# Kernel tuning notes

Hardware: AMD Instinct MI355X
Metric: run time of the kernel (lower is better)

The kernel has to match this reference:

```python
import jax, jax.numpy as jnp
import numpy as np
from jax.scipy.special import gammaln

LOG_PROBS_PRECISION = -1.0e5  # large negative log-prob for impossible obs under bookend state
N_STATES_TOTAL = 25           # 1 bookend + 24 NB states
N_SPOTS = 4_000_000
TOTAL_EXP_READ_DEPTH = 25.0


def setup_inputs() -> dict:
    key = jax.random.key(0)
    k1, k2, k3 = jax.random.split(key, 3)
    # init_emission: means = depth * rand, phis = rand
    state_means = TOTAL_EXP_READ_DEPTH * jax.random.uniform(k1, (N_STATES_TOTAL,), dtype=jnp.float32)
    state_phis = jax.random.uniform(k2, (N_STATES_TOTAL,), dtype=jnp.float32)
    obs = jax.random.randint(k3, (N_SPOTS,), 0, 50, dtype=jnp.int32)
    return {"state_means": state_means, "state_phis": state_phis, "obs": obs}


def reference(state_means, state_phis, obs):
    # obs: [S] int counts -> float for lgamma math
    x = obs.astype(jnp.float32)  # [S]
    # Bookend state (index 0): log_prob 0 where obs == 0, else LOG_PROBS_PRECISION
    bookend = jnp.where(obs > 0, jnp.float32(LOG_PROBS_PRECISION), jnp.float32(0.0))  # [S]
    # NB states 1..K: mean/overdispersion parameterization
    mu = state_means[1:, None]   # [K, 1]
    phi = state_phis[1:, None]   # [K, 1]
    nb = (gammaln(x[None, :] + phi) - gammaln(phi) - gammaln(x[None, :] + 1.0)
          + phi * jnp.log(phi / (phi + mu))
          + x[None, :] * jnp.log(mu / (phi + mu)))  # [K, S]
    return jnp.concatenate([bookend[None, :], nb], axis=0)  # [K+1, S]
```

## Files before the change

### kernel.cpp

```cpp
#include <hip/hip_runtime.h>
#include <hip/hip_bf16.h>

#define N_STATES 25
#define N_XVALS  50
#define TBL_SZ   (N_STATES * N_XVALS)
#define LOG_PROBS_PRECISION -100000.0f

typedef int   i32x4 __attribute__((ext_vector_type(4)));
typedef float f32x4 __attribute__((ext_vector_type(4)));

__global__ void build_table_kernel(const float* __restrict__ means,
                                   const float* __restrict__ phis,
                                   float* __restrict__ table) {
    int idx = blockIdx.x * blockDim.x + threadIdx.x;
    if (idx >= TBL_SZ) return;
    int s = idx / N_XVALS;
    int x = idx % N_XVALS;
    float v;
    if (s == 0) {
        v = (x > 0) ? LOG_PROBS_PRECISION : 0.0f;
    } else {
        float mu  = means[s];
        float phi = phis[s];
        float rising = 0.0f;
        for (int j = 0; j < x; ++j) rising += logf(phi + (float)j);
        float logfact = 0.0f;
        for (int j = 2; j <= x; ++j) logfact += logf((float)j);
        float c = phi * logf(phi / (phi + mu));
        float d = logf(mu  / (phi + mu));
        v = rising - logfact + c + (float)x * d;
    }
    table[idx] = v;
}

__global__ __launch_bounds__(256) void
emit_kernel(const int* __restrict__ obs,
            const float* __restrict__ table,
            float* __restrict__ out,
            int n_spots) {
    __shared__ float t[TBL_SZ];
    for (int i = threadIdx.x; i < TBL_SZ; i += 256) t[i] = table[i];
    __syncthreads();

    int g = blockIdx.x * 256 + threadIdx.x;
    if (g * 4 >= n_spots) return;

    i32x4 o = __builtin_nontemporal_load(((const i32x4*)obs) + g);
    int x0 = min(max(o.x, 0), N_XVALS - 1);
    int x1 = min(max(o.y, 0), N_XVALS - 1);
    int x2 = min(max(o.z, 0), N_XVALS - 1);
    int x3 = min(max(o.w, 0), N_XVALS - 1);

#pragma unroll
    for (int s = 0; s < N_STATES; ++s) {
        const float* row = t + s * N_XVALS;
        f32x4 v;
        v.x = row[x0];
        v.y = row[x1];
        v.z = row[x2];
        v.w = row[x3];
        f32x4* dst = ((f32x4*)(out + (size_t)s * (size_t)n_spots)) + g;
        __builtin_nontemporal_store(v, dst);
    }
}

extern "C" void kernel_launch(void* const* d_in, const int* in_sizes, int n_in,
                              void* d_out, int out_size, void* d_ws, size_t ws_size,
                              hipStream_t stream) {
    const float* means = (const float*)d_in[0];
    const float* phis  = (const float*)d_in[1];
    const int*   obs   = (const int*)d_in[2];
    float* out = (float*)d_out;
    float* table = (float*)d_ws;

    int n_spots = in_sizes[2];

    build_table_kernel<<<(TBL_SZ + 255) / 256, 256, 0, stream>>>(means, phis, table);

    int groups = n_spots / 4;
    int blocks = (groups + 255) / 256;
    emit_kernel<<<blocks, 256, 0, stream>>>(obs, table, out, n_spots);
}
```

Before: 414.4 us.

## Split emission gather into per-state grid rows, each block writing one output row

The emit kernel now uses a 2D grid with one grid row per state, so each block writes a contiguous chunk of a single output row. Each block handles 1024 groups of four spots and loads only its 50-entry table row into shared memory. The goal is more streaming, locality-friendly writes and a smaller shared-memory footprint. In exchange, obs is read 25 times instead of once (about 400 MB of output plus repeated 16 MB input reads), and the nontemporal load hint on obs is dropped so those reads can hit in cache.

```diff
diff --git a/kernel.cpp b/kernel.cpp
--- a/kernel.cpp
+++ b/kernel.cpp
@@ -5,6 +5,7 @@
 #define N_XVALS  50
 #define TBL_SZ   (N_STATES * N_XVALS)
 #define LOG_PROBS_PRECISION -100000.0f
+#define GROUPS_PER_BLOCK 1024
 
 typedef int   i32x4 __attribute__((ext_vector_type(4)));
 typedef float f32x4 __attribute__((ext_vector_type(4)));
@@ -34,33 +35,31 @@
 }
 
 __global__ __launch_bounds__(256) void
-emit_kernel(const int* __restrict__ obs,
-            const float* __restrict__ table,
-            float* __restrict__ out,
-            int n_spots) {
-    __shared__ float t[TBL_SZ];
-    for (int i = threadIdx.x; i < TBL_SZ; i += 256) t[i] = table[i];
+emit_row_kernel(const int* __restrict__ obs,
+                const float* __restrict__ table,
+                float* __restrict__ out,
+                int n_groups, int n_spots) {
+    const int s = blockIdx.y;
+    __shared__ float row[N_XVALS];
+    if (threadIdx.x < N_XVALS) row[threadIdx.x] = table[s * N_XVALS + threadIdx.x];
     __syncthreads();
 
-    int g = blockIdx.x * 256 + threadIdx.x;
-    if (g * 4 >= n_spots) return;
-
-    i32x4 o = __builtin_nontemporal_load(((const i32x4*)obs) + g);
-    int x0 = min(max(o.x, 0), N_XVALS - 1);
-    int x1 = min(max(o.y, 0), N_XVALS - 1);
-    int x2 = min(max(o.z, 0), N_XVALS - 1);
-    int x3 = min(max(o.w, 0), N_XVALS - 1);
+    f32x4* dst = (f32x4*)(out + (size_t)s * (size_t)n_spots);
+    const i32x4* src = (const i32x4*)obs;
+    int base = blockIdx.x * GROUPS_PER_BLOCK + threadIdx.x;
 
 #pragma unroll
-    for (int s = 0; s < N_STATES; ++s) {
-        const float* row = t + s * N_XVALS;
-        f32x4 v;
-        v.x = row[x0];
-        v.y = row[x1];
-        v.z = row[x2];
-        v.w = row[x3];
-        f32x4* dst = ((f32x4*)(out + (size_t)s * (size_t)n_spots)) + g;
-        __builtin_nontemporal_store(v, dst);
+    for (int k = 0; k < 4; ++k) {
+        int g = base + k * 256;
+        if (g < n_groups) {
+            i32x4 o = src[g];
+            f32x4 v;
+            v.x = row[min(max(o.x, 0), N_XVALS - 1)];
+            v.y = row[min(max(o.y, 0), N_XVALS - 1)];
+            v.z = row[min(max(o.z, 0), N_XVALS - 1)];
+            v.w = row[min(max(o.w, 0), N_XVALS - 1)];
+            __builtin_nontemporal_store(v, dst + g);
+        }
     }
 }
 
@@ -73,11 +72,11 @@
     float* out = (float*)d_out;
     float* table = (float*)d_ws;
 
-    int n_spots = in_sizes[2];
+    int n_spots  = in_sizes[2];
+    int n_groups = n_spots / 4;
 
     build_table_kernel<<<(TBL_SZ + 255) / 256, 256, 0, stream>>>(means, phis, table);
 
-    int groups = n_spots / 4;
-    int blocks = (groups + 255) / 256;
-    emit_kernel<<<blocks, 256, 0, stream>>>(obs, table, out, n_spots);
+    dim3 grid((n_groups + GROUPS_PER_BLOCK - 1) / GROUPS_PER_BLOCK, N_STATES);
+    emit_row_kernel<<<grid, 256, 0, stream>>>(obs, table, out, n_groups, n_spots);
 }
```

Measured after the change: 450.6 us. 1.09x slower.
